# Performance work log

Hardware: AMD Instinct MI355X
Metric: run time of the kernel (lower is better)

## Reference

```python
import jax, jax.numpy as jnp
import numpy as np

# CIN config: input_dim (num_fields) = 32, cross_layer_sizes = [128, 128, 128], split_half = True
NUM_FIELDS = 32
EMBED_DIM = 16
BATCH = 4096
CROSS_SIZES = [128, 128, 128]


def setup_inputs() -> dict:
    key = jax.random.key(0)
    ks = jax.random.split(key, 8)
    x = jax.random.normal(ks[0], (BATCH, NUM_FIELDS, EMBED_DIM), dtype=jnp.float32)
    # Conv1d(kernel_size=1) weights: (out_ch, in_ch) + bias (out_ch,)
    prev = NUM_FIELDS
    inp = {"x": x}
    for i, cs in enumerate(CROSS_SIZES):
        in_ch = NUM_FIELDS * prev
        scale = 1.0 / np.sqrt(in_ch)
        inp[f"W{i}"] = jax.random.uniform(ks[1 + 2 * i], (cs, in_ch), dtype=jnp.float32, minval=-scale, maxval=scale)
        inp[f"b{i}"] = jax.random.uniform(ks[2 + 2 * i], (cs,), dtype=jnp.float32, minval=-scale, maxval=scale)
        prev = cs // 2  # split_half (applied after all but last, but prev for next conv uses halved size)
    return inp


def _cin_forward(x, Ws, bs):
    # x: (B, F, E)
    x0 = x
    h = x
    xs = []
    n_layers = len(Ws)
    for i in range(n_layers):
        B, F, E = x0.shape
        G = h.shape[1]
        # outer product over field dims -> (B, F*G, E)
        z = (x0[:, :, None, :] * h[:, None, :, :]).reshape(B, F * G, E)
        # 1x1 conv == channel matmul; bias broadcast over embed dim; relu
        y = jax.nn.relu(jnp.einsum('oc,bce->boe', Ws[i], z) + bs[i][None, :, None])
        if i != n_layers - 1:
            half = y.shape[1] // 2
            x_keep, h = y[:, :half, :], y[:, half:, :]
        else:
            x_keep, h = y, y
        xs.append(x_keep)
    return jnp.sum(jnp.concatenate(xs, axis=1), axis=2)  # (B, fc_input_dim)


def reference(x, W0, b0, W1, b1, W2, b2):
    return _cin_forward(x, [W0, W1, W2], [b0, b1, b2])
```

## Files before the change

kernel.cpp:

```cpp
#include <hip/hip_runtime.h>

typedef _Float16 half_t;
typedef _Float16 v8h __attribute__((ext_vector_type(8)));
typedef float v4f __attribute__((ext_vector_type(4)));

#define XTP 40
#define HP  72

typedef __attribute__((address_space(3))) unsigned int lds_u32;
typedef const __attribute__((address_space(1))) unsigned int glb_u32;

__device__ __forceinline__ void dma16(const half_t* g, half_t* l, int lane) {
  __builtin_amdgcn_global_load_lds((glb_u32*)(g + lane * 8), (lds_u32*)(l), 16, 0, 0);
}

#define WAITVM(N) __builtin_amdgcn_s_waitcnt(0xF70 | (N))
#define SCHED0()  __builtin_amdgcn_sched_barrier(0)

__global__ __launch_bounds__(256) void prep_w_all(const float* __restrict__ W0,
                                                  const float* __restrict__ W1,
                                                  const float* __restrict__ W2,
                                                  half_t* __restrict__ w0h,
                                                  half_t* __restrict__ w1h,
                                                  half_t* __restrict__ w2h) {
  int i = blockIdx.x * 256 + threadIdx.x;
  const float* src; half_t* dst; int ktot; int ksh; int j;
  if (i < 16384)      { src = W0; dst = w0h; ktot = 1024; ksh = 7; j = i; }
  else if (i < 49152) { src = W1; dst = w1h; ktot = 2048; ksh = 8; j = i - 16384; }
  else                { src = W2; dst = w2h; ktot = 2048; ksh = 8; j = i - 49152; }
  int o = j >> ksh, k8 = j & ((1 << ksh) - 1);
  const float* s = src + (size_t)o * ktot + k8 * 8;
  float4 f0 = *(const float4*)s;
  float4 f1 = *(const float4*)(s + 4);
  union { half_t h[8]; uint4 u; } pk;
  pk.h[0] = (half_t)f0.x; pk.h[1] = (half_t)f0.y; pk.h[2] = (half_t)f0.z; pk.h[3] = (half_t)f0.w;
  pk.h[4] = (half_t)f1.x; pk.h[5] = (half_t)f1.y; pk.h[6] = (half_t)f1.z; pk.h[7] = (half_t)f1.w;
  *(uint4*)(dst + ((size_t)k8 * 128 + o) * 8) = pk.u;
}

template <int G, int KTOT, int KEEP, int OUT_BASE, bool H_OUT, bool H_IS_X>
__device__ __forceinline__ void layer(const half_t* __restrict__ wgt,
                                      const float* __restrict__ bias,
                                      half_t* __restrict__ xt_lds,
                                      half_t* __restrict__ h_lds,
                                      half_t* __restrict__ w_ring,
                                      float* __restrict__ out,
                                      size_t b0, int tid, int phase) {
  constexpr int SPO = (G == 64) ? 16 : 8;
  constexpr int NOCT = (KTOT / 32) / SPO;
  constexpr int NSEL = (G == 64) ? 2 : 1;
  const int lane = tid & 63;
  const int wv = tid >> 6;
  const int wm = (wv & 3) * 32;
  const int wb = (wv >> 2) * 4;
  const int col = lane & 15;
  const int kq = lane >> 4;

  int lrow[4];
#pragma unroll
  for (int ni = 0; ni < 4; ++ni) lrow[ni] = (wb + ni) * 16 + col;

  __syncthreads();

  const half_t* hb = H_IS_X ? xt_lds : h_lds;
  const int hpitch = H_IS_X ? XTP : HP;
  v8h hreg[4][NSEL];
#pragma unroll
  for (int ni = 0; ni < 4; ++ni) {
    const half_t* hp = hb + lrow[ni] * hpitch + kq * 8;
    hreg[ni][0] = *(const v8h*)hp;
    if (NSEL > 1) hreg[ni][NSEL - 1] = *(const v8h*)(hp + 32);
  }

#pragma unroll
  for (int p = 0; p < 3; ++p) {
    const half_t* wsrc = wgt + (size_t)(phase * SPO + p) * 4096;
    dma16(wsrc + wv * 512, w_ring + p * 4096 + wv * 512, lane);
  }
  __syncthreads();

  v4f acc[2][4] = {};

#pragma unroll 1
  for (int oi = 0; oi < NOCT - 1; ++oi) {
    const int oct_a = (oi + phase) & 3;
    const int next_a = (oi + 1 + phase) & 3;
    v8h xv[4];
#pragma unroll
    for (int ni = 0; ni < 4; ++ni)
      xv[ni] = *(const v8h*)(xt_lds + lrow[ni] * XTP + oct_a * 8);
#pragma unroll
    for (int t = 0; t < SPO; ++t) {
      SCHED0(); WAITVM(2); __builtin_amdgcn_s_barrier(); SCHED0();
      {
        const int tp = t + 3;
        const half_t* wsrc = (tp < SPO)
            ? wgt + (size_t)(oct_a * SPO + tp) * 4096
            : wgt + (size_t)(next_a * SPO + (tp - SPO)) * 4096;
        dma16(wsrc + wv * 512, w_ring + (tp & 3) * 4096 + wv * 512, lane);
      }
      const half_t* rb = w_ring + (t & 3) * 4096;
      const int j = (G == 64) ? (t >> 1) : t;
      const int sel = (G == 64) ? (t & 1) : 0;
      v8h a0 = *(const v8h*)(rb + (kq * 128 + wm + col) * 8);
      v8h a1 = *(const v8h*)(rb + (kq * 128 + wm + 16 + col) * 8);
#pragma unroll
      for (int ni = 0; ni < 4; ++ni) {
        v8h bfr = hreg[ni][sel] * xv[ni][j];
        acc[0][ni] = __builtin_amdgcn_mfma_f32_16x16x32_f16(a0, bfr, acc[0][ni], 0, 0, 0);
        acc[1][ni] = __builtin_amdgcn_mfma_f32_16x16x32_f16(a1, bfr, acc[1][ni], 0, 0, 0);
      }
    }
  }

  {
    const int oct_a = (NOCT - 1 + phase) & 3;
    v8h xv[4];
#pragma unroll
    for (int ni = 0; ni < 4; ++ni)
      xv[ni] = *(const v8h*)(xt_lds + lrow[ni] * XTP + oct_a * 8);
#pragma unroll
    for (int t = 0; t < SPO; ++t) {
      SCHED0();
      if (t < SPO - 2) { WAITVM(2); } else if (t == SPO - 2) { WAITVM(1); } else { WAITVM(0); }
      __builtin_amdgcn_s_barrier(); SCHED0();
      if (t + 3 < SPO) {
        const int tp = t + 3;
        const half_t* wsrc = wgt + (size_t)(oct_a * SPO + tp) * 4096;
        dma16(wsrc + wv * 512, w_ring + (tp & 3) * 4096 + wv * 512, lane);
      }
      const half_t* rb = w_ring + (t & 3) * 4096;
      const int j = (G == 64) ? (t >> 1) : t;
      const int sel = (G == 64) ? (t & 1) : 0;
      v8h a0 = *(const v8h*)(rb + (kq * 128 + wm + col) * 8);
      v8h a1 = *(const v8h*)(rb + (kq * 128 + wm + 16 + col) * 8);
#pragma unroll
      for (int ni = 0; ni < 4; ++ni) {
        v8h bfr = hreg[ni][sel] * xv[ni][j];
        acc[0][ni] = __builtin_amdgcn_mfma_f32_16x16x32_f16(a0, bfr, acc[0][ni], 0, 0, 0);
        acc[1][ni] = __builtin_amdgcn_mfma_f32_16x16x32_f16(a1, bfr, acc[1][ni], 0, 0, 0);
      }
    }
  }

#pragma unroll
  for (int mi = 0; mi < 2; ++mi) {
    const int o_base = wm + mi * 16 + kq * 4;
    float4 b4 = *(const float4*)(bias + o_base);
#pragma unroll
    for (int ni = 0; ni < 4; ++ni) {
      const int bb = wb + ni;
      float v[4];
#pragma unroll
      for (int r = 0; r < 4; ++r)
        v[r] = fmaxf(acc[mi][ni][r] + (&b4.x)[r], 0.0f);
      if (H_OUT && o_base >= 64) {
        union { half_t h[4]; uint2 u; } pk;
#pragma unroll
        for (int r = 0; r < 4; ++r) pk.h[r] = (half_t)v[r];
        *(uint2*)(h_lds + (bb * 16 + col) * HP + (o_base - 64)) = pk.u;
      }
      if (o_base < KEEP) {
#pragma unroll
        for (int r = 0; r < 4; ++r) {
          float sv = v[r];
          sv += __shfl_xor(sv, 1);
          sv += __shfl_xor(sv, 2);
          sv += __shfl_xor(sv, 4);
          sv += __shfl_xor(sv, 8);
          if (col == 0) out[(b0 + bb) * 256 + OUT_BASE + o_base + r] = sv;
        }
      }
    }
  }
}

__global__ __launch_bounds__(512, 4) void cin_fused(const float* __restrict__ x,
                                                    const half_t* __restrict__ w0h,
                                                    const half_t* __restrict__ w1h,
                                                    const half_t* __restrict__ w2h,
                                                    const float* __restrict__ b0p,
                                                    const float* __restrict__ b1p,
                                                    const float* __restrict__ b2p,
                                                    float* __restrict__ out) {
  __shared__ __align__(16) half_t xt_lds[128 * XTP];
  __shared__ __align__(16) half_t h_lds[128 * HP];
  __shared__ __align__(16) half_t w_ring[4 * 4096];

  const int tid = threadIdx.x;
  const size_t b0 = (size_t)blockIdx.x * 8;
  const int phase = (blockIdx.x >> 3) & 3;

#pragma unroll
  for (int i = 0; i < 2; ++i) {
    int idx = (i * 512 + tid) * 4;
    float4 v = *(const float4*)(x + b0 * 512 + idx);
    int e = idx & 15, f = (idx >> 4) & 31, b = idx >> 9;
    half_t* d = xt_lds + (b * 16 + e) * XTP + f;
    d[0 * XTP] = (half_t)v.x;
    d[1 * XTP] = (half_t)v.y;
    d[2 * XTP] = (half_t)v.z;
    d[3 * XTP] = (half_t)v.w;
  }

  layer<32, 1024, 64, 0, true, true>(w0h, b0p, xt_lds, h_lds, w_ring, out, b0, tid, phase);
  layer<64, 2048, 64, 64, true, false>(w1h, b1p, xt_lds, h_lds, w_ring, out, b0, tid, phase);
  layer<64, 2048, 128, 128, false, false>(w2h, b2p, xt_lds, h_lds, w_ring, out, b0, tid, phase);
}

extern "C" void kernel_launch(void* const* d_in, const int* in_sizes, int n_in,
                              void* d_out, int out_size, void* d_ws, size_t ws_size,
                              hipStream_t stream) {
  const float* x  = (const float*)d_in[0];
  const float* W0 = (const float*)d_in[1];
  const float* b0 = (const float*)d_in[2];
  const float* W1 = (const float*)d_in[3];
  const float* b1 = (const float*)d_in[4];
  const float* W2 = (const float*)d_in[5];
  const float* b2 = (const float*)d_in[6];
  float* out = (float*)d_out;
  char* ws = (char*)d_ws;

  half_t* w0h = (half_t*)(ws);
  half_t* w1h = (half_t*)(ws + (256u << 10));
  half_t* w2h = (half_t*)(ws + (768u << 10));

  prep_w_all<<<320, 256, 0, stream>>>(W0, W1, W2, w0h, w1h, w2h);
  cin_fused<<<512, 512, 0, stream>>>(x, w0h, w1h, w2h, b0, b1, b2, out);
}
```

Measured before the change: 153.9 us.

## Switch CIN layer GEMM to 32x32x16 MFMA with 3-slot double-step weight ring

Replaces the 16x16x32 MFMA tiling with 32x32x16 MFMA. Each wave now covers a 32-output by 32-column tile (two batch rows stacked), which changes the fragment and register layout and the epilogue indexing. The weight ring becomes three 8192-element slots that each hold two K-steps, prefetched two steps ahead. This halves the number of barriers per layer and raises MFMA work per A-fragment load. The costs are more LDS for the ring and a different accumulator layout, which must map correctly to the h_lds writes and the output reductions.

```diff
diff --git a/kernel.cpp b/kernel.cpp
--- a/kernel.cpp
+++ b/kernel.cpp
@@ -2,7 +2,7 @@
 
 typedef _Float16 half_t;
 typedef _Float16 v8h __attribute__((ext_vector_type(8)));
-typedef float v4f __attribute__((ext_vector_type(4)));
+typedef float f32x16 __attribute__((ext_vector_type(16)));
 
 #define XTP 40
 #define HP  72
@@ -46,121 +46,133 @@
                                       half_t* __restrict__ w_ring,
                                       float* __restrict__ out,
                                       size_t b0, int tid, int phase) {
-  constexpr int SPO = (G == 64) ? 16 : 8;
-  constexpr int NOCT = (KTOT / 32) / SPO;
-  constexpr int NSEL = (G == 64) ? 2 : 1;
+  constexpr int SPO = (G == 64) ? 8 : 4;
+  constexpr int NG  = G / 16;
   const int lane = tid & 63;
   const int wv = tid >> 6;
   const int wm = (wv & 3) * 32;
   const int wb = (wv >> 2) * 4;
-  const int col = lane & 15;
-  const int kq = lane >> 4;
-
-  int lrow[4];
-#pragma unroll
-  for (int ni = 0; ni < 4; ++ni) lrow[ni] = (wb + ni) * 16 + col;
+  const int e16 = lane & 15;
+  const int col32 = lane & 31;
+  const int bsel = (lane >> 4) & 1;
+  const int khi = lane >> 5;
+
+  int lrow[2];
+#pragma unroll
+  for (int ni = 0; ni < 2; ++ni) lrow[ni] = (wb + ni * 2 + bsel) * 16 + e16;
 
   __syncthreads();
 
   const half_t* hb = H_IS_X ? xt_lds : h_lds;
   const int hpitch = H_IS_X ? XTP : HP;
-  v8h hreg[4][NSEL];
-#pragma unroll
-  for (int ni = 0; ni < 4; ++ni) {
-    const half_t* hp = hb + lrow[ni] * hpitch + kq * 8;
-    hreg[ni][0] = *(const v8h*)hp;
-    if (NSEL > 1) hreg[ni][NSEL - 1] = *(const v8h*)(hp + 32);
-  }
-
-#pragma unroll
-  for (int p = 0; p < 3; ++p) {
-    const half_t* wsrc = wgt + (size_t)(phase * SPO + p) * 4096;
-    dma16(wsrc + wv * 512, w_ring + p * 4096 + wv * 512, lane);
+  v8h hreg[2][NG];
+#pragma unroll
+  for (int ni = 0; ni < 2; ++ni)
+#pragma unroll
+    for (int gi = 0; gi < NG; ++gi)
+      hreg[ni][gi] = *(const v8h*)(hb + lrow[ni] * hpitch + gi * 16 + khi * 8);
+
+  const int oct0 = phase & 3;
+#pragma unroll
+  for (int p = 0; p < 2; ++p) {
+    const half_t* ws = wgt + (size_t)(oct0 * 2 * SPO + 2 * p) * 4096 + wv * 512;
+    dma16(ws,        w_ring + p * 8192 + wv * 512, lane);
+    dma16(ws + 4096, w_ring + p * 8192 + 4096 + wv * 512, lane);
   }
   __syncthreads();
 
-  v4f acc[2][4] = {};
+  f32x16 acc[2] = {};
+  int cur = 0, prv = 2;
+
+  const half_t* rbl = w_ring + khi * 1024 + (wm + col32) * 8;
 
 #pragma unroll 1
-  for (int oi = 0; oi < NOCT - 1; ++oi) {
-    const int oct_a = (oi + phase) & 3;
-    const int next_a = (oi + 1 + phase) & 3;
-    v8h xv[4];
-#pragma unroll
-    for (int ni = 0; ni < 4; ++ni)
-      xv[ni] = *(const v8h*)(xt_lds + lrow[ni] * XTP + oct_a * 8);
+  for (int oi = 0; oi < 3; ++oi) {
+    const int oct = (oi + phase) & 3;
+    const int nxt = (oi + 1 + phase) & 3;
+    v8h xv[2];
+#pragma unroll
+    for (int ni = 0; ni < 2; ++ni)
+      xv[ni] = *(const v8h*)(xt_lds + lrow[ni] * XTP + oct * 8);
 #pragma unroll
     for (int t = 0; t < SPO; ++t) {
       SCHED0(); WAITVM(2); __builtin_amdgcn_s_barrier(); SCHED0();
       {
-        const int tp = t + 3;
-        const half_t* wsrc = (tp < SPO)
-            ? wgt + (size_t)(oct_a * SPO + tp) * 4096
-            : wgt + (size_t)(next_a * SPO + (tp - SPO)) * 4096;
-        dma16(wsrc + wv * 512, w_ring + (tp & 3) * 4096 + wv * 512, lane);
-      }
-      const half_t* rb = w_ring + (t & 3) * 4096;
-      const int j = (G == 64) ? (t >> 1) : t;
-      const int sel = (G == 64) ? (t & 1) : 0;
-      v8h a0 = *(const v8h*)(rb + (kq * 128 + wm + col) * 8);
-      v8h a1 = *(const v8h*)(rb + (kq * 128 + wm + 16 + col) * 8);
-#pragma unroll
-      for (int ni = 0; ni < 4; ++ni) {
-        v8h bfr = hreg[ni][sel] * xv[ni][j];
-        acc[0][ni] = __builtin_amdgcn_mfma_f32_16x16x32_f16(a0, bfr, acc[0][ni], 0, 0, 0);
-        acc[1][ni] = __builtin_amdgcn_mfma_f32_16x16x32_f16(a1, bfr, acc[1][ni], 0, 0, 0);
-      }
+        const int tp = t + 2;
+        const half_t* ws = (tp < SPO)
+            ? wgt + (size_t)(oct * 2 * SPO + 2 * tp) * 4096
+            : wgt + (size_t)(nxt * 2 * SPO + 2 * (tp - SPO)) * 4096;
+        dma16(ws + wv * 512,        w_ring + prv * 8192 + wv * 512, lane);
+        dma16(ws + 4096 + wv * 512, w_ring + prv * 8192 + 4096 + wv * 512, lane);
+      }
+      const half_t* rb = rbl + cur * 8192;
+#pragma unroll
+      for (int s = 0; s < 2; ++s)
+#pragma unroll
+        for (int m = 0; m < 2; ++m) {
+          v8h a = *(const v8h*)(rb + s * 4096 + m * 2048);
+#pragma unroll
+          for (int ni = 0; ni < 2; ++ni) {
+            v8h bfr = (G == 64) ? hreg[ni][s * 2 + m] * xv[ni][t]
+                                : hreg[ni][m] * xv[ni][2 * t + s];
+            acc[ni] = __builtin_amdgcn_mfma_f32_32x32x16_f16(a, bfr, acc[ni], 0, 0, 0);
+          }
+        }
+      const int nx = 3 - cur - prv; prv = cur; cur = nx;
     }
   }
 
   {
-    const int oct_a = (NOCT - 1 + phase) & 3;
-    v8h xv[4];
-#pragma unroll
-    for (int ni = 0; ni < 4; ++ni)
-      xv[ni] = *(const v8h*)(xt_lds + lrow[ni] * XTP + oct_a * 8);
+    const int oct = (3 + phase) & 3;
+    v8h xv[2];
+#pragma unroll
+    for (int ni = 0; ni < 2; ++ni)
+      xv[ni] = *(const v8h*)(xt_lds + lrow[ni] * XTP + oct * 8);
 #pragma unroll
     for (int t = 0; t < SPO; ++t) {
       SCHED0();
-      if (t < SPO - 2) { WAITVM(2); } else if (t == SPO - 2) { WAITVM(1); } else { WAITVM(0); }
+      if (t < SPO - 1) { WAITVM(2); } else { WAITVM(0); }
       __builtin_amdgcn_s_barrier(); SCHED0();
-      if (t + 3 < SPO) {
-        const int tp = t + 3;
-        const half_t* wsrc = wgt + (size_t)(oct_a * SPO + tp) * 4096;
-        dma16(wsrc + wv * 512, w_ring + (tp & 3) * 4096 + wv * 512, lane);
-      }
-      const half_t* rb = w_ring + (t & 3) * 4096;
-      const int j = (G == 64) ? (t >> 1) : t;
-      const int sel = (G == 64) ? (t & 1) : 0;
-      v8h a0 = *(const v8h*)(rb + (kq * 128 + wm + col) * 8);
-      v8h a1 = *(const v8h*)(rb + (kq * 128 + wm + 16 + col) * 8);
-#pragma unroll
-      for (int ni = 0; ni < 4; ++ni) {
-        v8h bfr = hreg[ni][sel] * xv[ni][j];
-        acc[0][ni] = __builtin_amdgcn_mfma_f32_16x16x32_f16(a0, bfr, acc[0][ni], 0, 0, 0);
-        acc[1][ni] = __builtin_amdgcn_mfma_f32_16x16x32_f16(a1, bfr, acc[1][ni], 0, 0, 0);
-      }
+      if (t + 2 < SPO) {
+        const half_t* ws = wgt + (size_t)(oct * 2 * SPO + 2 * (t + 2)) * 4096;
+        dma16(ws + wv * 512,        w_ring + prv * 8192 + wv * 512, lane);
+        dma16(ws + 4096 + wv * 512, w_ring + prv * 8192 + 4096 + wv * 512, lane);
+      }
+      const half_t* rb = rbl + cur * 8192;
+#pragma unroll
+      for (int s = 0; s < 2; ++s)
+#pragma unroll
+        for (int m = 0; m < 2; ++m) {
+          v8h a = *(const v8h*)(rb + s * 4096 + m * 2048);
+#pragma unroll
+          for (int ni = 0; ni < 2; ++ni) {
+            v8h bfr = (G == 64) ? hreg[ni][s * 2 + m] * xv[ni][t]
+                                : hreg[ni][m] * xv[ni][2 * t + s];
+            acc[ni] = __builtin_amdgcn_mfma_f32_32x32x16_f16(a, bfr, acc[ni], 0, 0, 0);
+          }
+        }
+      const int nx = 3 - cur - prv; prv = cur; cur = nx;
     }
   }
 
 #pragma unroll
-  for (int mi = 0; mi < 2; ++mi) {
-    const int o_base = wm + mi * 16 + kq * 4;
-    float4 b4 = *(const float4*)(bias + o_base);
-#pragma unroll
-    for (int ni = 0; ni < 4; ++ni) {
-      const int bb = wb + ni;
+  for (int ni = 0; ni < 2; ++ni) {
+    const int bb = wb + ni * 2 + bsel;
+#pragma unroll
+    for (int q = 0; q < 4; ++q) {
+      const int o_base = wm + khi * 4 + q * 8;
+      float4 b4 = *(const float4*)(bias + o_base);
       float v[4];
 #pragma unroll
       for (int r = 0; r < 4; ++r)
-        v[r] = fmaxf(acc[mi][ni][r] + (&b4.x)[r], 0.0f);
-      if (H_OUT && o_base >= 64) {
+        v[r] = fmaxf(acc[ni][q * 4 + r] + (&b4.x)[r], 0.0f);
+      if (H_OUT && wm >= 64) {
         union { half_t h[4]; uint2 u; } pk;
 #pragma unroll
         for (int r = 0; r < 4; ++r) pk.h[r] = (half_t)v[r];
-        *(uint2*)(h_lds + (bb * 16 + col) * HP + (o_base - 64)) = pk.u;
-      }
-      if (o_base < KEEP) {
+        *(uint2*)(h_lds + (bb * 16 + e16) * HP + (o_base - 64)) = pk.u;
+      }
+      if (wm < KEEP) {
 #pragma unroll
         for (int r = 0; r < 4; ++r) {
           float sv = v[r];
@@ -168,7 +180,7 @@
           sv += __shfl_xor(sv, 2);
           sv += __shfl_xor(sv, 4);
           sv += __shfl_xor(sv, 8);
-          if (col == 0) out[(b0 + bb) * 256 + OUT_BASE + o_base + r] = sv;
+          if (e16 == 0) out[(b0 + bb) * 256 + OUT_BASE + o_base + r] = sv;
         }
       }
     }
@@ -185,7 +197,7 @@
                                                     float* __restrict__ out) {
   __shared__ __align__(16) half_t xt_lds[128 * XTP];
   __shared__ __align__(16) half_t h_lds[128 * HP];
-  __shared__ __align__(16) half_t w_ring[4 * 4096];
+  __shared__ __align__(16) half_t w_ring[3 * 8192];
 
   const int tid = threadIdx.x;
   const size_t b0 = (size_t)blockIdx.x * 8;
```

Measured after the change: 159.6 us. 1.04x slower.

## Load weights directly from global into registers and halve per-block batch

Applied to the files above, without the earlier changes.

Drops the LDS weight ring that was filled by global_load_lds, along with its per-step barriers. Each wave now owns 16 output channels and streams its weight slice straight from global/L2 into registers using a two-deep software prefetch. The weight prep kernel writes a layout blocked by 16 output rows so each wave reads contiguous data. The batch per block falls from 8 to 4, doubling the grid to 1024 blocks, and the occupancy hint rises to 6. This removes barrier synchronisation and LDS traffic, but every wave now fetches weights separately, which multiplies L2 reads and exposes global latency behind a shallow prefetch.

```diff
diff --git a/kernel.cpp b/kernel.cpp
--- a/kernel.cpp
+++ b/kernel.cpp
@@ -6,16 +6,6 @@
 
 #define XTP 40
 #define HP  72
-
-typedef __attribute__((address_space(3))) unsigned int lds_u32;
-typedef const __attribute__((address_space(1))) unsigned int glb_u32;
-
-__device__ __forceinline__ void dma16(const half_t* g, half_t* l, int lane) {
-  __builtin_amdgcn_global_load_lds((glb_u32*)(g + lane * 8), (lds_u32*)(l), 16, 0, 0);
-}
-
-#define WAITVM(N) __builtin_amdgcn_s_waitcnt(0xF70 | (N))
-#define SCHED0()  __builtin_amdgcn_sched_barrier(0)
 
 __global__ __launch_bounds__(256) void prep_w_all(const float* __restrict__ W0,
                                                   const float* __restrict__ W1,
@@ -35,147 +25,119 @@
   union { half_t h[8]; uint4 u; } pk;
   pk.h[0] = (half_t)f0.x; pk.h[1] = (half_t)f0.y; pk.h[2] = (half_t)f0.z; pk.h[3] = (half_t)f0.w;
   pk.h[4] = (half_t)f1.x; pk.h[5] = (half_t)f1.y; pk.h[6] = (half_t)f1.z; pk.h[7] = (half_t)f1.w;
-  *(uint4*)(dst + ((size_t)k8 * 128 + o) * 8) = pk.u;
+  size_t di = ((size_t)(((o >> 4) << ksh) + k8) * 128) + (size_t)(o & 15) * 8;
+  *(uint4*)(dst + di) = pk.u;
 }
 
 template <int G, int KTOT, int KEEP, int OUT_BASE, bool H_OUT, bool H_IS_X>
 __device__ __forceinline__ void layer(const half_t* __restrict__ wgt,
                                       const float* __restrict__ bias,
-                                      half_t* __restrict__ xt_lds,
+                                      const half_t* __restrict__ xt_lds,
                                       half_t* __restrict__ h_lds,
-                                      half_t* __restrict__ w_ring,
                                       float* __restrict__ out,
-                                      size_t b0, int tid, int phase) {
-  constexpr int SPO = (G == 64) ? 16 : 8;
-  constexpr int NOCT = (KTOT / 32) / SPO;
+                                      size_t b0, int tid) {
+  constexpr int SPO  = (G == 64) ? 16 : 8;
   constexpr int NSEL = (G == 64) ? 2 : 1;
   const int lane = tid & 63;
   const int wv = tid >> 6;
-  const int wm = (wv & 3) * 32;
-  const int wb = (wv >> 2) * 4;
-  const int col = lane & 15;
+  const int e16 = lane & 15;
   const int kq = lane >> 4;
+
+  __syncthreads();
 
   int lrow[4];
 #pragma unroll
-  for (int ni = 0; ni < 4; ++ni) lrow[ni] = (wb + ni) * 16 + col;
-
-  __syncthreads();
+  for (int ni = 0; ni < 4; ++ni) lrow[ni] = ni * 16 + e16;
 
   const half_t* hb = H_IS_X ? xt_lds : h_lds;
   const int hpitch = H_IS_X ? XTP : HP;
   v8h hreg[4][NSEL];
 #pragma unroll
-  for (int ni = 0; ni < 4; ++ni) {
-    const half_t* hp = hb + lrow[ni] * hpitch + kq * 8;
-    hreg[ni][0] = *(const v8h*)hp;
-    if (NSEL > 1) hreg[ni][NSEL - 1] = *(const v8h*)(hp + 32);
-  }
+  for (int ni = 0; ni < 4; ++ni)
+#pragma unroll
+    for (int s = 0; s < NSEL; ++s)
+      hreg[ni][s] = *(const v8h*)(hb + lrow[ni] * hpitch + s * 32 + kq * 8);
 
-#pragma unroll
-  for (int p = 0; p < 3; ++p) {
-    const half_t* wsrc = wgt + (size_t)(phase * SPO + p) * 4096;
-    dma16(wsrc + wv * 512, w_ring + p * 4096 + wv * 512, lane);
-  }
   __syncthreads();
 
-  v4f acc[2][4] = {};
+  const half_t* wl = wgt + (size_t)wv * (KTOT * 16) + kq * 128 + e16 * 8;
+  v8h a_cur = *(const v8h*)(wl);
+  v8h a_nxt = *(const v8h*)(wl + 512);
+  wl += 1024;
+
+  v4f acc[4] = {};
+  v8h xv[4];
+
+  auto step = [&](v8h a, int t) {
+    const int j   = (G == 64) ? (t >> 1) : t;
+    const int sel = (G == 64) ? (t & 1) : 0;
+#pragma unroll
+    for (int ni = 0; ni < 4; ++ni) {
+      v8h bfr = hreg[ni][sel] * xv[ni][j];
+      acc[ni] = __builtin_amdgcn_mfma_f32_16x16x32_f16(a, bfr, acc[ni], 0, 0, 0);
+    }
+  };
 
 #pragma unroll 1
-  for (int oi = 0; oi < NOCT - 1; ++oi) {
-    const int oct_a = (oi + phase) & 3;
-    const int next_a = (oi + 1 + phase) & 3;
-    v8h xv[4];
+  for (int oct = 0; oct < 3; ++oct) {
 #pragma unroll
     for (int ni = 0; ni < 4; ++ni)
-      xv[ni] = *(const v8h*)(xt_lds + lrow[ni] * XTP + oct_a * 8);
+      xv[ni] = *(const v8h*)(xt_lds + lrow[ni] * XTP + oct * 8);
 #pragma unroll
-    for (int t = 0; t < SPO; ++t) {
-      SCHED0(); WAITVM(2); __builtin_amdgcn_s_barrier(); SCHED0();
-      {
-        const int tp = t + 3;
-        const half_t* wsrc = (tp < SPO)
-            ? wgt + (size_t)(oct_a * SPO + tp) * 4096
-            : wgt + (size_t)(next_a * SPO + (tp - SPO)) * 4096;
-        dma16(wsrc + wv * 512, w_ring + (tp & 3) * 4096 + wv * 512, lane);
-      }
-      const half_t* rb = w_ring + (t & 3) * 4096;
-      const int j = (G == 64) ? (t >> 1) : t;
-      const int sel = (G == 64) ? (t & 1) : 0;
-      v8h a0 = *(const v8h*)(rb + (kq * 128 + wm + col) * 8);
-      v8h a1 = *(const v8h*)(rb + (kq * 128 + wm + 16 + col) * 8);
-#pragma unroll
-      for (int ni = 0; ni < 4; ++ni) {
-        v8h bfr = hreg[ni][sel] * xv[ni][j];
-        acc[0][ni] = __builtin_amdgcn_mfma_f32_16x16x32_f16(a0, bfr, acc[0][ni], 0, 0, 0);
-        acc[1][ni] = __builtin_amdgcn_mfma_f32_16x16x32_f16(a1, bfr, acc[1][ni], 0, 0, 0);
-      }
+    for (int t = 0; t < SPO; t += 2) {
+      v8h a0 = a_cur; a_cur = *(const v8h*)(wl);
+      step(a0, t);
+      v8h a1 = a_nxt; a_nxt = *(const v8h*)(wl + 512);
+      wl += 1024;
+      step(a1, t + 1);
     }
   }
 
   {
-    const int oct_a = (NOCT - 1 + phase) & 3;
-    v8h xv[4];
 #pragma unroll
     for (int ni = 0; ni < 4; ++ni)
-      xv[ni] = *(const v8h*)(xt_lds + lrow[ni] * XTP + oct_a * 8);
+      xv[ni] = *(const v8h*)(xt_lds + lrow[ni] * XTP + 3 * 8);
 #pragma unroll
-    for (int t = 0; t < SPO; ++t) {
-      SCHED0();
-      if (t < SPO - 2) { WAITVM(2); } else if (t == SPO - 2) { WAITVM(1); } else { WAITVM(0); }
-      __builtin_amdgcn_s_barrier(); SCHED0();
-      if (t + 3 < SPO) {
-        const int tp = t + 3;
-        const half_t* wsrc = wgt + (size_t)(oct_a * SPO + tp) * 4096;
-        dma16(wsrc + wv * 512, w_ring + (tp & 3) * 4096 + wv * 512, lane);
-      }
-      const half_t* rb = w_ring + (t & 3) * 4096;
-      const int j = (G == 64) ? (t >> 1) : t;
-      const int sel = (G == 64) ? (t & 1) : 0;
-      v8h a0 = *(const v8h*)(rb + (kq * 128 + wm + col) * 8);
-      v8h a1 = *(const v8h*)(rb + (kq * 128 + wm + 16 + col) * 8);
-#pragma unroll
-      for (int ni = 0; ni < 4; ++ni) {
-        v8h bfr = hreg[ni][sel] * xv[ni][j];
-        acc[0][ni] = __builtin_amdgcn_mfma_f32_16x16x32_f16(a0, bfr, acc[0][ni], 0, 0, 0);
-        acc[1][ni] = __builtin_amdgcn_mfma_f32_16x16x32_f16(a1, bfr, acc[1][ni], 0, 0, 0);
-      }
+    for (int t = 0; t < SPO - 2; t += 2) {
+      v8h a0 = a_cur; a_cur = *(const v8h*)(wl);
+      step(a0, t);
+      v8h a1 = a_nxt; a_nxt = *(const v8h*)(wl + 512);
+      wl += 1024;
+      step(a1, t + 1);
     }
+    step(a_cur, SPO - 2);
+    step(a_nxt, SPO - 1);
   }
 
+  const int o_base = wv * 16 + kq * 4;
+  float4 b4 = *(const float4*)(bias + o_base);
 #pragma unroll
-  for (int mi = 0; mi < 2; ++mi) {
-    const int o_base = wm + mi * 16 + kq * 4;
-    float4 b4 = *(const float4*)(bias + o_base);
+  for (int ni = 0; ni < 4; ++ni) {
+    float v[4];
 #pragma unroll
-    for (int ni = 0; ni < 4; ++ni) {
-      const int bb = wb + ni;
-      float v[4];
+    for (int r = 0; r < 4; ++r)
+      v[r] = fmaxf(acc[ni][r] + (&b4.x)[r], 0.0f);
+    if (H_OUT && wv >= 4) {
+      union { half_t h[4]; uint2 u; } pk;
 #pragma unroll
-      for (int r = 0; r < 4; ++r)
-        v[r] = fmaxf(acc[mi][ni][r] + (&b4.x)[r], 0.0f);
-      if (H_OUT && o_base >= 64) {
-        union { half_t h[4]; uint2 u; } pk;
+      for (int r = 0; r < 4; ++r) pk.h[r] = (half_t)v[r];
+      *(uint2*)(h_lds + lrow[ni] * HP + (o_base - 64)) = pk.u;
+    }
+    if (wv * 16 < KEEP) {
 #pragma unroll
-        for (int r = 0; r < 4; ++r) pk.h[r] = (half_t)v[r];
-        *(uint2*)(h_lds + (bb * 16 + col) * HP + (o_base - 64)) = pk.u;
-      }
-      if (o_base < KEEP) {
-#pragma unroll
-        for (int r = 0; r < 4; ++r) {
-          float sv = v[r];
-          sv += __shfl_xor(sv, 1);
-          sv += __shfl_xor(sv, 2);
-          sv += __shfl_xor(sv, 4);
-          sv += __shfl_xor(sv, 8);
-          if (col == 0) out[(b0 + bb) * 256 + OUT_BASE + o_base + r] = sv;
-        }
+      for (int r = 0; r < 4; ++r) {
+        float sv = v[r];
+        sv += __shfl_xor(sv, 1);
+        sv += __shfl_xor(sv, 2);
+        sv += __shfl_xor(sv, 4);
+        sv += __shfl_xor(sv, 8);
+        if (e16 == 0) out[(b0 + ni) * 256 + OUT_BASE + o_base + r] = sv;
       }
     }
   }
 }
 
-__global__ __launch_bounds__(512, 4) void cin_fused(const float* __restrict__ x,
+__global__ __launch_bounds__(512, 6) void cin_fused(const float* __restrict__ x,
                                                     const half_t* __restrict__ w0h,
                                                     const half_t* __restrict__ w1h,
                                                     const half_t* __restrict__ w2h,
@@ -183,17 +145,14 @@
                                                     const float* __restrict__ b1p,
                                                     const float* __restrict__ b2p,
                                                     float* __restrict__ out) {
-  __shared__ __align__(16) half_t xt_lds[128 * XTP];
-  __shared__ __align__(16) half_t h_lds[128 * HP];
-  __shared__ __align__(16) half_t w_ring[4 * 4096];
+  __shared__ __align__(16) half_t xt_lds[64 * XTP];
+  __shared__ __align__(16) half_t h_lds[64 * HP];
 
   const int tid = threadIdx.x;
-  const size_t b0 = (size_t)blockIdx.x * 8;
-  const int phase = (blockIdx.x >> 3) & 3;
+  const size_t b0 = (size_t)blockIdx.x * 4;
 
-#pragma unroll
-  for (int i = 0; i < 2; ++i) {
-    int idx = (i * 512 + tid) * 4;
+  {
+    int idx = tid * 4;
     float4 v = *(const float4*)(x + b0 * 512 + idx);
     int e = idx & 15, f = (idx >> 4) & 31, b = idx >> 9;
     half_t* d = xt_lds + (b * 16 + e) * XTP + f;
@@ -203,9 +162,9 @@
     d[3 * XTP] = (half_t)v.w;
   }
 
-  layer<32, 1024, 64, 0, true, true>(w0h, b0p, xt_lds, h_lds, w_ring, out, b0, tid, phase);
-  layer<64, 2048, 64, 64, true, false>(w1h, b1p, xt_lds, h_lds, w_ring, out, b0, tid, phase);
-  layer<64, 2048, 128, 128, false, false>(w2h, b2p, xt_lds, h_lds, w_ring, out, b0, tid, phase);
+  layer<32, 1024, 64, 0, true, true>(w0h, b0p, xt_lds, h_lds, out, b0, tid);
+  layer<64, 2048, 64, 64, true, false>(w1h, b1p, xt_lds, h_lds, out, b0, tid);
+  layer<64, 2048, 128, 128, false, false>(w2h, b2p, xt_lds, h_lds, out, b0, tid);
 }
 
 extern "C" void kernel_launch(void* const* d_in, const int* in_sizes, int n_in,
@@ -226,5 +185,5 @@
   half_t* w2h = (half_t*)(ws + (768u << 10));
 
   prep_w_all<<<320, 256, 0, stream>>>(W0, W1, W2, w0h, w1h, w2h);
-  cin_fused<<<512, 512, 0, stream>>>(x, w0h, w1h, w2h, b0, b1, b2, out);
+  cin_fused<<<1024, 512, 0, stream>>>(x, w0h, w1h, w2h, b0, b1, b2, out);
 }
```

Measured after the change: 240.6 us. +56.3%, slower.
